# Kernel optimization log

Measured on AMD Instinct MI355X. Metric: run time of the kernel, lower is better.

## Reference

```python
import jax, jax.numpy as jnp
import numpy as np

HEAD_DIM = 64
HIDDEN_SIZE = 2880
NUM_HEADS = 64
NUM_KV_HEADS = 8
INPUT_SIZE = 2 * HIDDEN_SIZE


def _rotate_half(x):
    x1, x2 = jnp.split(x, 2, axis=-1)
    return jnp.concatenate([-x2, x1], axis=-1)


def _apply_rotary_emb(x, cos, sin):
    return x * cos + _rotate_half(x) * sin


def setup_inputs() -> dict:
    key = jax.random.key(0)
    ks = jax.random.split(key, 7)
    B, S = 1, 2048
    hidden_states = jax.random.normal(ks[0], (B, S, INPUT_SIZE), dtype=jnp.float32)
    cos = jax.random.uniform(ks[1], (1, 1, S, HEAD_DIM), dtype=jnp.float32)
    sin = jax.random.uniform(ks[2], (1, 1, S, HEAD_DIM), dtype=jnp.float32)
    sc = 1.0 / np.sqrt(INPUT_SIZE)
    wq = jax.random.normal(ks[3], (INPUT_SIZE, NUM_HEADS * HEAD_DIM), dtype=jnp.float32) * sc
    wk = jax.random.normal(ks[4], (INPUT_SIZE, NUM_KV_HEADS * HEAD_DIM), dtype=jnp.float32) * sc
    wv = jax.random.normal(ks[5], (INPUT_SIZE, NUM_KV_HEADS * HEAD_DIM), dtype=jnp.float32) * sc
    wo = jax.random.normal(ks[6], (NUM_HEADS * HEAD_DIM, HIDDEN_SIZE), dtype=jnp.float32) * (1.0 / np.sqrt(NUM_HEADS * HEAD_DIM))
    return {"hidden_states": hidden_states, "cos": cos, "sin": sin,
            "wq": wq, "wk": wk, "wv": wv, "wo": wo}


def reference(hidden_states, cos, sin, wq, wk, wv, wo):
    B, S, _ = hidden_states.shape
    # projections -> [B, H, S, D]
    q = (hidden_states @ wq).reshape(B, S, NUM_HEADS, HEAD_DIM).transpose(0, 2, 1, 3)
    k = (hidden_states @ wk).reshape(B, S, NUM_KV_HEADS, HEAD_DIM).transpose(0, 2, 1, 3)
    v = (hidden_states @ wv).reshape(B, S, NUM_KV_HEADS, HEAD_DIM).transpose(0, 2, 1, 3)
    q = _apply_rotary_emb(q, cos, sin)
    k = _apply_rotary_emb(k, cos, sin)
    # GQA expand KV heads: [B, Hkv, S, D] -> [B, H, S, D]
    groups = NUM_HEADS // NUM_KV_HEADS
    k = jnp.repeat(k, groups, axis=1)
    v = jnp.repeat(v, groups, axis=1)
    scale = 1.0 / np.sqrt(HEAD_DIM).astype(np.float32)
    attn = jnp.einsum('bhqd,bhkd->bhqk', q, k) * scale  # [B,H,S,S]
    attn = jax.nn.softmax(attn.astype(jnp.float32), axis=-1).astype(q.dtype)
    out = jnp.einsum('bhqk,bhkd->bhqd', attn, v)
    out = out.transpose(0, 2, 1, 3).reshape(B, S, NUM_HEADS * HEAD_DIM)
    return out @ wo
```

## Files before the change

### kernel.cpp

```cpp
#include <hip/hip_runtime.h>
#include <hip/hip_bf16.h>

#define SEQ   2048
#define INSZ  5760
#define NQ    4096
#define NKV   512
#define NQKV  5120
#define HQ    64
#define HKV   8
#define HD    64
#define HID   2880
#define HIDP  2944

typedef __attribute__((ext_vector_type(8))) short bf16x8;
typedef __attribute__((ext_vector_type(4))) float f32x4;
typedef __attribute__((ext_vector_type(16))) float f32x16;
typedef unsigned int u32;

__device__ __forceinline__ unsigned short f2bf(float x) {
  __hip_bfloat16 b = __float2bfloat16(x);
  return __builtin_bit_cast(unsigned short, b);
}
__device__ __forceinline__ float bf2f(unsigned short u) {
  return __bfloat162float(__builtin_bit_cast(__hip_bfloat16, u));
}
__device__ __forceinline__ float exp2_hw(float x) {
  float r;
  asm("v_exp_f32 %0, %1" : "=v"(r) : "v"(x));
  return r;
}
__device__ __forceinline__ u32 cvt_pk_bf16(float lo, float hi) {
  u32 r;
  asm("v_cvt_pk_bf16_f32 %0, %1, %2" : "=v"(r) : "v"(lo), "v"(hi));
  return r;
}

__global__ void k_convert(const float* __restrict__ src, unsigned short* __restrict__ dst, int n) {
  int stride = gridDim.x * blockDim.x * 4;
  for (int idx = (blockIdx.x * blockDim.x + threadIdx.x) * 4; idx < n; idx += stride) {
    float4 v = *(const float4*)(src + idx);
    ushort4 o;
    o.x = f2bf(v.x); o.y = f2bf(v.y); o.z = f2bf(v.z); o.w = f2bf(v.w);
    *(ushort4*)(dst + idx) = o;
  }
}

__global__ void k_tconv(const float* __restrict__ src, unsigned short* __restrict__ dst,
                        int K, int N) {
  __shared__ float tile[32][33];
  int k0 = blockIdx.x * 32, n0 = blockIdx.y * 32;
  int r = threadIdx.x >> 5, c = threadIdx.x & 31;
#pragma unroll
  for (int i = 0; i < 4; i++) {
    int row = i * 8 + r;
    float v = (n0 + c < N) ? src[(size_t)(k0 + row) * N + n0 + c] : 0.f;
    tile[row][c] = v;
  }
  __syncthreads();
#pragma unroll
  for (int i = 0; i < 4; i++) {
    int n = n0 + i * 8 + r;
    dst[(size_t)n * K + k0 + c] = f2bf(tile[c][i * 8 + r]);
  }
}

template <typename OutT>
__global__ __launch_bounds__(256) void k_gemm_bt(
    const unsigned short* __restrict__ A,
    const unsigned short* __restrict__ BT,
    OutT* __restrict__ C, int Kdim, int Ncols, int ldc) {
  __shared__ unsigned short sA[128 * 32];
  __shared__ unsigned short sB[128 * 32];
  int tid = threadIdx.x, wid = tid >> 6, lane = tid & 63;
  int gx = gridDim.x;
  int nwg = gx * gridDim.y;
  int lin = blockIdx.y * gx + blockIdx.x;
  int qn = nwg >> 3, rn = nwg & 7;
  int xcd = lin & 7, idx = lin >> 3;
  int swz = (xcd < rn ? xcd * (qn + 1) : rn * (qn + 1) + (xcd - rn) * qn) + idx;
  int bm = swz % gx, bn = swz / gx;
  const unsigned short* Ab = A + (size_t)bm * 128 * Kdim;
  const unsigned short* Bb = BT + (size_t)bn * 128 * Kdim;
  f32x4 acc[4][4];
#pragma unroll
  for (int i = 0; i < 4; i++)
#pragma unroll
    for (int j = 0; j < 4; j++) acc[i][j] = f32x4{0.f, 0.f, 0.f, 0.f};
  int wr = (wid >> 1) * 64, wc = (wid & 1) * 64;
  int srow = lane >> 2;
  int selem = (lane & 3) * 8;
  int rbase = lane & 15, koff = (lane >> 4) * 8;

  for (int kt = 0; kt < Kdim; kt += 32) {
    __syncthreads();
#pragma unroll
    for (int ch2 = 0; ch2 < 2; ++ch2) {
      int chunk = wid * 2 + ch2;
      const unsigned short* ga = Ab + (size_t)(chunk * 16 + srow) * Kdim + kt + selem;
      const unsigned short* gb = Bb + (size_t)(chunk * 16 + srow) * Kdim + kt + selem;
      __builtin_amdgcn_global_load_lds(
          (const __attribute__((address_space(1))) void*)ga,
          (__attribute__((address_space(3))) void*)(sA + chunk * 512), 16, 0, 0);
      __builtin_amdgcn_global_load_lds(
          (const __attribute__((address_space(1))) void*)gb,
          (__attribute__((address_space(3))) void*)(sB + chunk * 512), 16, 0, 0);
    }
    __syncthreads();
    bf16x8 a[4], b[4];
#pragma unroll
    for (int i = 0; i < 4; i++)
      a[i] = *(const bf16x8*)(sA + (wr + i * 16 + rbase) * 32 + koff);
#pragma unroll
    for (int j = 0; j < 4; j++)
      b[j] = *(const bf16x8*)(sB + (wc + j * 16 + rbase) * 32 + koff);
#pragma unroll
    for (int i = 0; i < 4; i++)
#pragma unroll
      for (int j = 0; j < 4; j++)
        acc[i][j] = __builtin_amdgcn_mfma_f32_16x16x32_bf16(a[i], b[j], acc[i][j], 0, 0, 0);
  }
  int rw = (lane >> 4) * 4, cl = lane & 15;
#pragma unroll
  for (int i = 0; i < 4; i++)
#pragma unroll
    for (int j = 0; j < 4; j++) {
      int col = bn * 128 + wc + j * 16 + cl;
      if (col < Ncols) {
#pragma unroll
        for (int r = 0; r < 4; r++) {
          int row = bm * 128 + wr + i * 16 + rw + r;
          float v = acc[i][j][r];
          if constexpr (sizeof(OutT) == 2)
            C[(size_t)row * ldc + col] = (OutT)f2bf(v);
          else
            C[(size_t)row * ldc + col] = v;
        }
      }
    }
}

__global__ void k_rope(unsigned short* __restrict__ qkv, const float* __restrict__ cosb,
                       const float* __restrict__ sinb) {
  int s = blockIdx.x;
  const float* cs = cosb + s * HD;
  const float* sn = sinb + s * HD;
  unsigned short* row = qkv + (size_t)s * NQKV;
  for (int idx = threadIdx.x; idx < (HQ + HKV) * 32; idx += blockDim.x) {
    int head = idx >> 5, dp = idx & 31;
    unsigned short* base = row + (head < HQ ? head * 64 : NQ + (head - HQ) * 64);
    float x1 = bf2f(base[dp]), x2 = bf2f(base[dp + 32]);
    float o1 = x1 * cs[dp] - x2 * sn[dp];
    float o2 = x2 * cs[dp + 32] + x1 * sn[dp + 32];
    base[dp] = f2bf(o1);
    base[dp + 32] = f2bf(o2);
  }
}

__global__ void k_vtrans(const unsigned short* __restrict__ qkv, unsigned short* __restrict__ vt) {
  __shared__ unsigned short tile[64 * 66];
  int st = blockIdx.x, hk = blockIdx.y;
  int s0 = st * 64, t = threadIdx.x;
#pragma unroll
  for (int i = 0; i < 16; i++) {
    int e = i * 256 + t;
    int sl = e >> 6, d = e & 63;
    tile[d * 66 + sl] = qkv[(size_t)(s0 + sl) * NQKV + NQ + NKV + hk * 64 + d];
  }
  __syncthreads();
#pragma unroll
  for (int i = 0; i < 16; i++) {
    int e = i * 256 + t;
    int d = e >> 6, sl = e & 63;
    vt[(size_t)(hk * 64 + d) * SEQ + s0 + sl] = tile[d * 66 + sl];
  }
}

__global__ __launch_bounds__(256) void k_attn(
    const unsigned short* __restrict__ qkv, const unsigned short* __restrict__ vt,
    unsigned short* __restrict__ out) {
  __shared__ unsigned short smem[16384];
  int tid = threadIdx.x, wid = tid >> 6, lane = tid & 63;
  int head = blockIdx.x, qt = blockIdx.y;
  int hkv = head >> 3;
  int q = lane & 31, h = lane >> 5;
  int q0w = qt * 128 + wid * 32;
  const float SL2 = 0.125f * 1.44269504f;

  bf16x8 qf[4];
  {
    const unsigned short* qrow = qkv + (size_t)(q0w + q) * NQKV + head * 64 + h * 8;
#pragma unroll
    for (int ks = 0; ks < 4; ks++) qf[ks] = *(const bf16x8*)(qrow + ks * 16);
  }

  int r8 = lane >> 3;
  int srcslot = ((lane & 7) ^ r8) * 16;
  int sw = q & 7;

#define STAGE_KV(buf, kv)                                                            \
  {                                                                                  \
    _Pragma("unroll") for (int ch = 0; ch < 2; ++ch) {                               \
      int r0 = (wid * 2 + ch) * 8;                                                   \
      const char* gk =                                                               \
          (const char*)(qkv + (size_t)((kv) + r0 + r8) * NQKV + NQ + hkv * 64) +     \
          srcslot;                                                                   \
      __builtin_amdgcn_global_load_lds(                                              \
          (const __attribute__((address_space(1))) void*)gk,                         \
          (__attribute__((address_space(3))) void*)(smem + (buf)*4096 + r0 * 64),    \
          16, 0, 0);                                                                 \
      const char* gv =                                                               \
          (const char*)(vt + (size_t)(hkv * 64 + r0 + r8) * SEQ + (kv)) + srcslot;   \
      __builtin_amdgcn_global_load_lds(                                              \
          (const __attribute__((address_space(1))) void*)gv,                         \
          (__attribute__((address_space(3))) void*)(smem + 8192 + (buf)*4096 +       \
                                                    r0 * 64),                        \
          16, 0, 0);                                                                 \
    }                                                                                \
  }

  f32x16 o0, o1;
#pragma unroll
  for (int r = 0; r < 16; r++) { o0[r] = 0.f; o1[r] = 0.f; }
  float m = -3e38f, lp = 0.f;

  STAGE_KV(0, 0);
  __syncthreads();
  int cur = 0;

  for (int kvt = 0; kvt < SEQ / 64; ++kvt) {
    if (kvt + 1 < SEQ / 64) STAGE_KV(cur ^ 1, (kvt + 1) * 64);
    const char* kb = (const char*)(smem + cur * 4096);
    const char* vb = (const char*)(smem + 8192 + cur * 4096);

    f32x16 st0, st1;
#pragma unroll
    for (int r = 0; r < 16; r++) { st0[r] = 0.f; st1[r] = 0.f; }
    {
      bf16x8 kf[4];
#pragma unroll
      for (int ks = 0; ks < 4; ks++)
        kf[ks] = *(const bf16x8*)(kb + q * 128 + (((2 * ks + h) ^ sw) << 4));
#pragma unroll
      for (int ks = 0; ks < 4; ks++)
        st0 = __builtin_amdgcn_mfma_f32_32x32x16_bf16(kf[ks], qf[ks], st0, 0, 0, 0);
#pragma unroll
      for (int ks = 0; ks < 4; ks++)
        kf[ks] = *(const bf16x8*)(kb + (32 + q) * 128 + (((2 * ks + h) ^ sw) << 4));
#pragma unroll
      for (int ks = 0; ks < 4; ks++)
        st1 = __builtin_amdgcn_mfma_f32_32x32x16_bf16(kf[ks], qf[ks], st1, 0, 0, 0);
    }

    float tmx[16];
#pragma unroll
    for (int r = 0; r < 16; r++) tmx[r] = fmaxf(st0[r], st1[r]);
#pragma unroll
    for (int s = 8; s >= 1; s >>= 1)
#pragma unroll
      for (int r = 0; r < 8; r++)
        if (r < s) tmx[r] = fmaxf(tmx[r], tmx[r + s]);
    float mx = fmaxf(tmx[0], __shfl_xor(tmx[0], 32, 64));
    float t2 = mx * SL2;

    if (__any(t2 > m + 8.f)) {
      float mn = fmaxf(m, t2);
      float corr = exp2_hw(m - mn);
      m = mn;
      lp *= corr;
#pragma unroll
      for (int r = 0; r < 16; r++) { o0[r] *= corr; o1[r] *= corr; }
    }

    float psa[4] = {0.f, 0.f, 0.f, 0.f};
#pragma unroll
    for (int r = 0; r < 16; r++) {
      float e0 = exp2_hw(fmaf(st0[r], SL2, -m));
      float e1 = exp2_hw(fmaf(st1[r], SL2, -m));
      st0[r] = e0; st1[r] = e1;
      psa[r & 3] += e0 + e1;
    }
    lp += (psa[0] + psa[1]) + (psa[2] + psa[3]);

    u32 pk[16];
#pragma unroll
    for (int w = 0; w < 8; w++) {
      pk[w] = cvt_pk_bf16(st0[2 * w], st0[2 * w + 1]);
      pk[8 + w] = cvt_pk_bf16(st1[2 * w], st1[2 * w + 1]);
    }

    bf16x8 pf[4];
#pragma unroll
    for (int ks = 0; ks < 4; ks++) {
      int base = 8 * (ks >> 1) + 4 * (ks & 1);
      u32 wA0 = pk[base], wA1 = pk[base + 1], wB0 = pk[base + 2], wB1 = pk[base + 3];
      u32 keep0 = h ? wB0 : wA0, keep1 = h ? wB1 : wA1;
      u32 send0 = h ? wA0 : wB0, send1 = h ? wA1 : wB1;
      u32 rc0 = (u32)__shfl_xor((int)send0, 32, 64);
      u32 rc1 = (u32)__shfl_xor((int)send1, 32, 64);
      union { u32 w[4]; bf16x8 v; } u;
      u.w[0] = h ? rc0 : keep0;
      u.w[1] = h ? rc1 : keep1;
      u.w[2] = h ? keep0 : rc0;
      u.w[3] = h ? keep1 : rc1;
      pf[ks] = u.v;
    }

    {
      bf16x8 vf[4];
#pragma unroll
      for (int ks = 0; ks < 4; ks++)
        vf[ks] = *(const bf16x8*)(vb + q * 128 + (((2 * ks + h) ^ sw) << 4));
#pragma unroll
      for (int ks = 0; ks < 4; ks++)
        o0 = __builtin_amdgcn_mfma_f32_32x32x16_bf16(vf[ks], pf[ks], o0, 0, 0, 0);
#pragma unroll
      for (int ks = 0; ks < 4; ks++)
        vf[ks] = *(const bf16x8*)(vb + (32 + q) * 128 + (((2 * ks + h) ^ sw) << 4));
#pragma unroll
      for (int ks = 0; ks < 4; ks++)
        o1 = __builtin_amdgcn_mfma_f32_32x32x16_bf16(vf[ks], pf[ks], o1, 0, 0, 0);
    }

    __syncthreads();
    cur ^= 1;
  }

  float lpt = lp + __shfl_xor(lp, 32, 64);
  float inv = 1.0f / lpt;

  unsigned short* ot = smem + wid * (32 * 72);
#pragma unroll
  for (int w = 0; w < 8; w++) {
    int reg = 2 * w;
    int dbase = (reg & 3) + 8 * (reg >> 2) + 4 * h;
    u32 p0 = cvt_pk_bf16(o0[reg] * inv, o0[reg + 1] * inv);
    u32 p1 = cvt_pk_bf16(o1[reg] * inv, o1[reg + 1] * inv);
    *(u32*)(ot + q * 72 + dbase) = p0;
    *(u32*)(ot + q * 72 + 32 + dbase) = p1;
  }
  __syncthreads();
  int row = lane >> 1, halfc = lane & 1;
  const unsigned short* src = ot + row * 72 + halfc * 32;
  unsigned short* dst = out + (size_t)(q0w + row) * NQ + head * 64 + halfc * 32;
#pragma unroll
  for (int c = 0; c < 4; c++)
    *(bf16x8*)(dst + c * 8) = *(const bf16x8*)(src + c * 8);
#undef STAGE_KV
}

extern "C" void kernel_launch(void* const* d_in, const int* in_sizes, int n_in,
                              void* d_out, int out_size, void* d_ws, size_t ws_size,
                              hipStream_t stream) {
  const float* hidden = (const float*)d_in[0];
  const float* cosb = (const float*)d_in[1];
  const float* sinb = (const float*)d_in[2];
  const float* wq = (const float*)d_in[3];
  const float* wk = (const float*)d_in[4];
  const float* wv = (const float*)d_in[5];
  const float* wo = (const float*)d_in[6];
  float* out = (float*)d_out;

  unsigned short* hb = (unsigned short*)d_ws;
  unsigned short* qkv = hb + (size_t)SEQ * INSZ;
  unsigned short* wqkvT = qkv + (size_t)SEQ * NQKV;
  unsigned short* woT = wqkvT + (size_t)NQKV * INSZ;
  unsigned short* vt = woT + (size_t)HIDP * NQ;
  unsigned short* attn = vt + (size_t)NKV * SEQ;

  k_convert<<<dim3(1024), dim3(256), 0, stream>>>(hidden, hb, SEQ * INSZ);
  k_tconv<<<dim3(INSZ / 32, NQ / 32), dim3(256), 0, stream>>>(wq, wqkvT, INSZ, NQ);
  k_tconv<<<dim3(INSZ / 32, NKV / 32), dim3(256), 0, stream>>>(
      wk, wqkvT + (size_t)NQ * INSZ, INSZ, NKV);
  k_tconv<<<dim3(INSZ / 32, NKV / 32), dim3(256), 0, stream>>>(
      wv, wqkvT + (size_t)(NQ + NKV) * INSZ, INSZ, NKV);
  k_tconv<<<dim3(NQ / 32, HIDP / 32), dim3(256), 0, stream>>>(wo, woT, NQ, HID);

  k_gemm_bt<unsigned short><<<dim3(SEQ / 128, NQKV / 128), dim3(256), 0, stream>>>(
      hb, wqkvT, qkv, INSZ, NQKV, NQKV);
  k_rope<<<dim3(SEQ), dim3(256), 0, stream>>>(qkv, cosb, sinb);
  k_vtrans<<<dim3(SEQ / 64, HKV), dim3(256), 0, stream>>>(qkv, vt);
  k_attn<<<dim3(HQ, SEQ / 128), dim3(256), 0, stream>>>(qkv, vt, attn);
  k_gemm_bt<float><<<dim3(SEQ / 128, (HID + 127) / 128), dim3(256), 0, stream>>>(
      attn, woT, out, NQ, HID, HID);
}
```

Baseline: 673.1 us.

## Double-buffer GEMM LDS tiles and vectorize weight transpose-convert stores

The bf16 GEMM now uses two LDS buffers and issues the global-to-LDS loads for the next k-tile before computing on the current one, so there is one barrier per iteration instead of two. This is meant to overlap memory latency with MFMA work. The weight transpose/convert kernel now handles 64x32 tiles and writes packed 8-element bf16 vectors using v_cvt_pk_bf16, replacing scalar 2-byte stores. This doubles LDS use in the GEMM and depends on the async LDS loads having completed by the barrier.

```diff
diff --git a/kernel.cpp b/kernel.cpp
--- a/kernel.cpp
+++ b/kernel.cpp
@@ -47,21 +47,22 @@
 
 __global__ void k_tconv(const float* __restrict__ src, unsigned short* __restrict__ dst,
                         int K, int N) {
-  __shared__ float tile[32][33];
-  int k0 = blockIdx.x * 32, n0 = blockIdx.y * 32;
-  int r = threadIdx.x >> 5, c = threadIdx.x & 31;
-#pragma unroll
-  for (int i = 0; i < 4; i++) {
+  __shared__ float tile[64][33];
+  int k0 = blockIdx.x * 64, n0 = blockIdx.y * 32;
+  int tid = threadIdx.x;
+  int r = tid >> 5, c = tid & 31;
+#pragma unroll
+  for (int i = 0; i < 8; i++) {
     int row = i * 8 + r;
-    float v = (n0 + c < N) ? src[(size_t)(k0 + row) * N + n0 + c] : 0.f;
-    tile[row][c] = v;
-  }
-  __syncthreads();
-#pragma unroll
-  for (int i = 0; i < 4; i++) {
-    int n = n0 + i * 8 + r;
-    dst[(size_t)n * K + k0 + c] = f2bf(tile[c][i * 8 + r]);
-  }
+    tile[row][c] = (n0 + c < N) ? src[(size_t)(k0 + row) * N + n0 + c] : 0.f;
+  }
+  __syncthreads();
+  int n = tid >> 3, kk = (tid & 7) * 8;
+  union { u32 w[4]; bf16x8 v; } u;
+#pragma unroll
+  for (int j = 0; j < 4; j++)
+    u.w[j] = cvt_pk_bf16(tile[kk + 2 * j][n], tile[kk + 2 * j + 1][n]);
+  *(bf16x8*)(dst + (size_t)(n0 + n) * K + k0 + kk) = u.v;
 }
 
 template <typename OutT>
@@ -69,8 +70,8 @@
     const unsigned short* __restrict__ A,
     const unsigned short* __restrict__ BT,
     OutT* __restrict__ C, int Kdim, int Ncols, int ldc) {
-  __shared__ unsigned short sA[128 * 32];
-  __shared__ unsigned short sB[128 * 32];
+  __shared__ unsigned short sA[2][128 * 32];
+  __shared__ unsigned short sB[2][128 * 32];
   int tid = threadIdx.x, wid = tid >> 6, lane = tid & 63;
   int gx = gridDim.x;
   int nwg = gx * gridDim.y;
@@ -91,34 +92,43 @@
   int selem = (lane & 3) * 8;
   int rbase = lane & 15, koff = (lane >> 4) * 8;
 
-  for (int kt = 0; kt < Kdim; kt += 32) {
-    __syncthreads();
-#pragma unroll
-    for (int ch2 = 0; ch2 < 2; ++ch2) {
-      int chunk = wid * 2 + ch2;
-      const unsigned short* ga = Ab + (size_t)(chunk * 16 + srow) * Kdim + kt + selem;
-      const unsigned short* gb = Bb + (size_t)(chunk * 16 + srow) * Kdim + kt + selem;
-      __builtin_amdgcn_global_load_lds(
-          (const __attribute__((address_space(1))) void*)ga,
-          (__attribute__((address_space(3))) void*)(sA + chunk * 512), 16, 0, 0);
-      __builtin_amdgcn_global_load_lds(
-          (const __attribute__((address_space(1))) void*)gb,
-          (__attribute__((address_space(3))) void*)(sB + chunk * 512), 16, 0, 0);
-    }
-    __syncthreads();
+#define G_STAGE(buf, kt)                                                             \
+  {                                                                                  \
+    _Pragma("unroll") for (int ch2 = 0; ch2 < 2; ++ch2) {                            \
+      int chunk = wid * 2 + ch2;                                                     \
+      const unsigned short* ga = Ab + (size_t)(chunk * 16 + srow) * Kdim + (kt) + selem; \
+      const unsigned short* gb = Bb + (size_t)(chunk * 16 + srow) * Kdim + (kt) + selem; \
+      __builtin_amdgcn_global_load_lds(                                              \
+          (const __attribute__((address_space(1))) void*)ga,                         \
+          (__attribute__((address_space(3))) void*)(&sA[buf][chunk * 512]), 16, 0, 0); \
+      __builtin_amdgcn_global_load_lds(                                              \
+          (const __attribute__((address_space(1))) void*)gb,                         \
+          (__attribute__((address_space(3))) void*)(&sB[buf][chunk * 512]), 16, 0, 0); \
+    }                                                                                \
+  }
+
+  int nt = Kdim >> 5;
+  G_STAGE(0, 0);
+  __syncthreads();
+  int cur = 0;
+  for (int t = 0; t < nt; ++t) {
+    if (t + 1 < nt) G_STAGE(cur ^ 1, (t + 1) * 32);
     bf16x8 a[4], b[4];
 #pragma unroll
     for (int i = 0; i < 4; i++)
-      a[i] = *(const bf16x8*)(sA + (wr + i * 16 + rbase) * 32 + koff);
+      a[i] = *(const bf16x8*)(&sA[cur][(wr + i * 16 + rbase) * 32 + koff]);
 #pragma unroll
     for (int j = 0; j < 4; j++)
-      b[j] = *(const bf16x8*)(sB + (wc + j * 16 + rbase) * 32 + koff);
+      b[j] = *(const bf16x8*)(&sB[cur][(wc + j * 16 + rbase) * 32 + koff]);
 #pragma unroll
     for (int i = 0; i < 4; i++)
 #pragma unroll
       for (int j = 0; j < 4; j++)
         acc[i][j] = __builtin_amdgcn_mfma_f32_16x16x32_bf16(a[i], b[j], acc[i][j], 0, 0, 0);
-  }
+    __syncthreads();
+    cur ^= 1;
+  }
+#undef G_STAGE
   int rw = (lane >> 4) * 4, cl = lane & 15;
 #pragma unroll
   for (int i = 0; i < 4; i++)
@@ -368,12 +378,12 @@
   unsigned short* attn = vt + (size_t)NKV * SEQ;
 
   k_convert<<<dim3(1024), dim3(256), 0, stream>>>(hidden, hb, SEQ * INSZ);
-  k_tconv<<<dim3(INSZ / 32, NQ / 32), dim3(256), 0, stream>>>(wq, wqkvT, INSZ, NQ);
-  k_tconv<<<dim3(INSZ / 32, NKV / 32), dim3(256), 0, stream>>>(
+  k_tconv<<<dim3(INSZ / 64, NQ / 32), dim3(256), 0, stream>>>(wq, wqkvT, INSZ, NQ);
+  k_tconv<<<dim3(INSZ / 64, NKV / 32), dim3(256), 0, stream>>>(
       wk, wqkvT + (size_t)NQ * INSZ, INSZ, NKV);
-  k_tconv<<<dim3(INSZ / 32, NKV / 32), dim3(256), 0, stream>>>(
+  k_tconv<<<dim3(INSZ / 64, NKV / 32), dim3(256), 0, stream>>>(
       wv, wqkvT + (size_t)(NQ + NKV) * INSZ, INSZ, NKV);
-  k_tconv<<<dim3(NQ / 32, HIDP / 32), dim3(256), 0, stream>>>(wo, woT, NQ, HID);
+  k_tconv<<<dim3(NQ / 64, HIDP / 32), dim3(256), 0, stream>>>(wo, woT, NQ, HID);
 
   k_gemm_bt<unsigned short><<<dim3(SEQ / 128, NQKV / 128), dim3(256), 0, stream>>>(
       hb, wqkvT, qkv, INSZ, NQKV, NQKV);
```

Measured after the change: 624.7 us. 7.2% less time.
